# Kernel optimization log

Measured on AMD Instinct MI355X. Metric: run time of the kernel, lower is better.

## Reference

```python
import jax, jax.numpy as jnp
import numpy as np

B, S, D = 1, 2048, 1024
H, HD = 16, 64          # attention heads, head dim
DFF = 4096              # ffn hidden
IH, ID = 4, 64          # indexer heads / dim ('baseline' strategy)
TOP_K = 64
ROPE_BASE = 10000.0
LN_EPS = 1e-5


def setup_inputs() -> dict:
    key = jax.random.key(0)
    ks = jax.random.split(key, 12)
    g = lambda k, shape: (jax.random.normal(k, shape, dtype=jnp.float32) * 0.02)
    return {
        "x": jax.random.normal(ks[0], (B, S, D), dtype=jnp.float32),
        "w_qkv": g(ks[1], (D, 3 * D)),
        "w_o": g(ks[2], (D, D)),
        "ffn_w1": g(ks[3], (D, DFF)),
        "ffn_b1": jnp.zeros((DFF,), jnp.float32),
        "ffn_w2": g(ks[4], (DFF, D)),
        "ffn_b2": jnp.zeros((D,), jnp.float32),
        "ln1_g": jnp.ones((D,), jnp.float32),
        "ln1_b": jnp.zeros((D,), jnp.float32),
        "ln2_g": jnp.ones((D,), jnp.float32),
        "ln2_b": jnp.zeros((D,), jnp.float32),
        "idx_wq": g(ks[5], (D, IH * ID)),
        "idx_wk": g(ks[6], (D, ID)),
        "idx_ww": g(ks[7], (D, IH)),
    }


def _layernorm(x, g, b):
    m = jnp.mean(x, axis=-1, keepdims=True)
    v = jnp.var(x, axis=-1, keepdims=True)
    return (x - m) * jax.lax.rsqrt(v + LN_EPS) * g + b


def _rope(x):  # x: [B,S,H,HD], torchtune interleaved-pair convention
    half = HD // 2
    theta = 1.0 / (ROPE_BASE ** (jnp.arange(0, HD, 2, dtype=jnp.float32) / HD))  # [half]
    ang = jnp.arange(S, dtype=jnp.float32)[:, None] * theta                      # [S,half]
    cos = jnp.cos(ang)[None, :, None, :]
    sin = jnp.sin(ang)[None, :, None, :]
    xp = x.reshape(*x.shape[:-1], half, 2)
    x0, x1 = xp[..., 0], xp[..., 1]
    out = jnp.stack([x0 * cos - x1 * sin, x1 * cos + x0 * sin], axis=-1)
    return out.reshape(x.shape)


def reference(x, w_qkv, w_o, ffn_w1, ffn_b1, ffn_w2, ffn_b2,
              ln1_g, ln1_b, ln2_g, ln2_b, idx_wq, idx_wk, idx_ww):
    norm_x = _layernorm(x, ln1_g, ln1_b)

    qkv = norm_x @ w_qkv                              # [B,S,3D]
    q, k, v = jnp.split(qkv, 3, axis=-1)
    q = _rope(q.reshape(B, S, H, HD))
    k = _rope(k.reshape(B, S, H, HD))
    v = v.reshape(B, S, H, HD)

    # Lightning-style indexer: I[t,s] = sum_h w[t,h] * relu(q_i[t,h] . k_i[s])
    qi = (norm_x @ idx_wq).reshape(B, S, IH, ID)      # [B,S,IH,ID]
    ki = norm_x @ idx_wk                              # [B,S,ID]
    wi = norm_x @ idx_ww                              # [B,S,IH]
    qk = jnp.einsum("bthd,bsd->bths", qi, ki)         # [B,S,IH,S]
    index_scores = jnp.einsum("bth,bths->bts", wi, jax.nn.relu(qk))  # [B,S,S]

    # causal top-k token selection -> boolean mask
    causal = jnp.tril(jnp.ones((S, S), dtype=bool))
    masked_scores = jnp.where(causal, index_scores, -jnp.inf)
    _, topk_idx = jax.lax.top_k(masked_scores, TOP_K)  # [B,S,K]
    b_ix = jnp.arange(B)[:, None, None]
    q_ix = jnp.arange(S)[None, :, None]
    mask = jnp.zeros((B, S, S), dtype=bool).at[b_ix, q_ix, topk_idx].set(True)
    mask = mask & causal                               # [B,S,S]

    # masked SDPA
    logits = jnp.einsum("bqhd,bkhd->bhqk", q, k) / np.sqrt(HD)
    logits = jnp.where(mask[:, None, :, :], logits, -jnp.inf)
    attn = jax.nn.softmax(logits, axis=-1)
    attn_out = jnp.einsum("bhqk,bkhd->bqhd", attn, v).reshape(B, S, D)
    x = x + attn_out @ w_o

    h = _layernorm(x, ln2_g, ln2_b)
    ffn = jax.nn.gelu(h @ ffn_w1 + ffn_b1, approximate=False) @ ffn_w2 + ffn_b2
    return x + ffn
```

## Files before the change

### kernel.cpp

```cpp
#include <hip/hip_runtime.h>
#include <math.h>

#define S_LEN 2048
#define D_MODEL 1024
#define NHEAD 16
#define HDIM 64
#define DFF 4096
#define IH 4
#define IDM 64
#define TOPK 64
#define NIDX 336

typedef float f32x4 __attribute__((ext_vector_type(4)));
typedef short bf16x8 __attribute__((ext_vector_type(8)));

__device__ __forceinline__ unsigned short f2bf(float f) {
    unsigned u = __builtin_bit_cast(unsigned, f);
    u += 0x7fff + ((u >> 16) & 1);
    return (unsigned short)(u >> 16);
}
__device__ __forceinline__ float bf2f(unsigned short us) {
    return __builtin_bit_cast(float, (unsigned)us << 16);
}

__device__ __forceinline__ float gelu_exact(float v) {
    return 0.5f * v * (1.f + erff(v * 0.70710678118654752f));
}

__device__ __forceinline__ void gl_lds16(const void* g, void* l) {
    __builtin_amdgcn_global_load_lds(
        (const __attribute__((address_space(1))) void*)g,
        (__attribute__((address_space(3))) void*)l, 16, 0, 0);
}

__global__ __launch_bounds__(256) void ln_kernel(const float* __restrict__ x,
    const float* __restrict__ g, const float* __restrict__ b,
    float* __restrict__ outf, unsigned short* __restrict__ outb)
{
    int row = blockIdx.x, tid = threadIdx.x;
    const float4 v = *(const float4*)(x + (size_t)row * D_MODEL + tid * 4);
    float s = v.x + v.y + v.z + v.w;
    float ss = v.x * v.x + v.y * v.y + v.z * v.z + v.w * v.w;
    int lane = tid & 63, wv = tid >> 6;
    for (int o = 32; o; o >>= 1) { s += __shfl_xor(s, o); ss += __shfl_xor(ss, o); }
    __shared__ float rs[4], rss[4];
    if (lane == 0) { rs[wv] = s; rss[wv] = ss; }
    __syncthreads();
    float S = rs[0] + rs[1] + rs[2] + rs[3];
    float SS = rss[0] + rss[1] + rss[2] + rss[3];
    float mean = S * (1.f / D_MODEL);
    float var = SS * (1.f / D_MODEL) - mean * mean;
    float r = rsqrtf(var + 1e-5f);
    float4 gv = *(const float4*)(g + tid * 4);
    float4 bv = *(const float4*)(b + tid * 4);
    float4 o4;
    o4.x = (v.x - mean) * r * gv.x + bv.x;
    o4.y = (v.y - mean) * r * gv.y + bv.y;
    o4.z = (v.z - mean) * r * gv.z + bv.z;
    o4.w = (v.w - mean) * r * gv.w + bv.w;
    if (outf) *(float4*)(outf + (size_t)row * D_MODEL + tid * 4) = o4;
    if (outb) {
        ushort4 u4 = { f2bf(o4.x), f2bf(o4.y), f2bf(o4.z), f2bf(o4.w) };
        *(ushort4*)(outb + (size_t)row * D_MODEL + tid * 4) = u4;
    }
}

__global__ __launch_bounds__(256) void wtrans_kernel(const float* __restrict__ in,
    unsigned short* __restrict__ out, int K, int N)
{
    __shared__ float t[32][33];
    int k0 = blockIdx.y * 32, n0 = blockIdx.x * 32;
    int tid = threadIdx.x;
    int r = tid >> 5, c = tid & 31;
#pragma unroll
    for (int p = 0; p < 4; ++p)
        t[r + p * 8][c] = in[(size_t)(k0 + r + p * 8) * N + n0 + c];
    __syncthreads();
#pragma unroll
    for (int p = 0; p < 4; ++p)
        out[(size_t)(n0 + r + p * 8) * K + k0 + c] = f2bf(t[c][r + p * 8]);
}

__global__ __launch_bounds__(256) void wpack_kernel(const float* __restrict__ wq,
    const float* __restrict__ wk, const float* __restrict__ ww, float* __restrict__ Wc)
{
    int idx = blockIdx.x * 256 + threadIdx.x;
    if (idx >= D_MODEL * NIDX) return;
    int r = idx / NIDX, c = idx % NIDX;
    float v = 0.f;
    if (c < 256) v = wq[r * 256 + c];
    else if (c < 320) v = wk[r * 64 + (c - 256)];
    else if (c < 324) v = ww[r * 4 + (c - 320)];
    Wc[idx] = v;
}

__global__ __launch_bounds__(256) void gemm_bf16_n64(
    const unsigned short* __restrict__ A, const unsigned short* __restrict__ Bt,
    float* __restrict__ C, unsigned short* __restrict__ Cb,
    const float* __restrict__ bias, const float* __restrict__ R,
    int M, int N, int K, int act,
    float* __restrict__ P, int kchunk)
{
    __shared__ __attribute__((aligned(16))) unsigned short As[2][128 * 32];
    __shared__ __attribute__((aligned(16))) unsigned short Bs[2][64 * 32];
    int tid = threadIdx.x;
    int bm = blockIdx.y * 128, bn = blockIdx.x * 64;
    int wid = tid >> 6, lane = tid & 63;
    int wm = wid * 32;
    const unsigned short* Ab = A + (size_t)bm * K;
    const unsigned short* Bb = Bt + (size_t)bn * K;
    f32x4 acc[2][4];
#pragma unroll
    for (int i = 0; i < 2; ++i)
#pragma unroll
        for (int j = 0; j < 4; ++j)
            acc[i][j] = (f32x4){0.f, 0.f, 0.f, 0.f};

    int kbeg = blockIdx.z * kchunk;
    int kend = kbeg + kchunk;
    int fr = lane & 15;
    int srow = tid >> 2;
    int cels = (((tid & 3) ^ (srow & 3)) << 3);
    int dste = tid * 8;
    int selm = (((lane >> 4) ^ (fr & 3)) << 3);

    gl_lds16(Ab + (size_t)srow * K + kbeg + cels, &As[0][dste]);
    gl_lds16(Ab + (size_t)(srow + 64) * K + kbeg + cels, &As[0][dste + 2048]);
    gl_lds16(Bb + (size_t)srow * K + kbeg + cels, &Bs[0][dste]);
    __syncthreads();

    int cur = 0;
    for (int k0 = kbeg; k0 < kend; k0 += 32) {
        int nxt = k0 + 32;
        if (nxt < kend) {
            gl_lds16(Ab + (size_t)srow * K + nxt + cels, &As[cur ^ 1][dste]);
            gl_lds16(Ab + (size_t)(srow + 64) * K + nxt + cels, &As[cur ^ 1][dste + 2048]);
            gl_lds16(Bb + (size_t)srow * K + nxt + cels, &Bs[cur ^ 1][dste]);
        }
        bf16x8 af[2], bfv[4];
#pragma unroll
        for (int mi = 0; mi < 2; ++mi)
            af[mi] = *(const bf16x8*)&As[cur][(wm + mi * 16 + fr) * 32 + selm];
#pragma unroll
        for (int ni = 0; ni < 4; ++ni)
            bfv[ni] = *(const bf16x8*)&Bs[cur][(ni * 16 + fr) * 32 + selm];
#pragma unroll
        for (int mi = 0; mi < 2; ++mi)
#pragma unroll
            for (int ni = 0; ni < 4; ++ni)
                acc[mi][ni] = __builtin_amdgcn_mfma_f32_16x16x32_bf16(
                    af[mi], bfv[ni], acc[mi][ni], 0, 0, 0);
        __syncthreads();
        cur ^= 1;
    }
    int cl = lane & 15, rh = (lane >> 4) * 4;
    if (P) {
        float* Pz = P + (size_t)blockIdx.z * M * N;
#pragma unroll
        for (int mi = 0; mi < 2; ++mi)
#pragma unroll
            for (int ni = 0; ni < 4; ++ni) {
                int col = bn + ni * 16 + cl;
#pragma unroll
                for (int r = 0; r < 4; ++r) {
                    int row = bm + wm + mi * 16 + rh + r;
                    Pz[(size_t)row * N + col] = acc[mi][ni][r];
                }
            }
        return;
    }
#pragma unroll
    for (int mi = 0; mi < 2; ++mi) {
#pragma unroll
        for (int ni = 0; ni < 4; ++ni) {
            int col = bn + ni * 16 + cl;
            float bv = bias ? bias[col] : 0.f;
#pragma unroll
            for (int r = 0; r < 4; ++r) {
                int row = bm + wm + mi * 16 + rh + r;
                float v = acc[mi][ni][r] + bv;
                if (act) v = gelu_exact(v);
                size_t off = (size_t)row * N + col;
                if (R) v += R[off];
                if (C) C[off] = v;
                if (Cb) Cb[off] = f2bf(v);
            }
        }
    }
}

__global__ __launch_bounds__(256) void kreduce_kernel(const float* __restrict__ P,
    int nslice, float* __restrict__ C, const float* __restrict__ bias,
    const float* __restrict__ R, int M, int N)
{
    size_t total4 = (size_t)M * N / 4;
    size_t stride = (size_t)gridDim.x * 256;
    for (size_t i4 = blockIdx.x * 256 + threadIdx.x; i4 < total4; i4 += stride) {
        size_t off = i4 * 4;
        float4 v = *(const float4*)(P + off);
        for (int z = 1; z < nslice; ++z) {
            float4 p = *(const float4*)(P + (size_t)z * M * N + off);
            v.x += p.x; v.y += p.y; v.z += p.z; v.w += p.w;
        }
        if (bias) {
            float4 b4 = *(const float4*)(bias + (off % N));
            v.x += b4.x; v.y += b4.y; v.z += b4.z; v.w += b4.w;
        }
        if (R) {
            float4 r4 = *(const float4*)(R + off);
            v.x += r4.x; v.y += r4.y; v.z += r4.z; v.w += r4.w;
        }
        *(float4*)(C + off) = v;
    }
}

__global__ __launch_bounds__(256) void gemm64(const float* __restrict__ A,
    const float* __restrict__ B, float* __restrict__ C,
    int M, int N, int K,
    float* __restrict__ P, int kchunk)
{
    __shared__ float As[16][68];
    __shared__ float Bs[16][68];
    int tid = threadIdx.x;
    int bm = blockIdx.y, bn = blockIdx.x;
    int tx = tid & 15, ty = tid >> 4;
    int arow = tid >> 2;
    int acol = (tid & 3) << 2;
    int brow = tid >> 4;
    int bcol = (tid & 15) << 2;
    const float* Abase = A + (size_t)(bm * 64 + arow) * K + acol;
    float c[4][4] = {};
    int kbeg = blockIdx.z * kchunk;
    int kend = kbeg + kchunk;
    for (int k0 = kbeg; k0 < kend; k0 += 16) {
        float4 av = *(const float4*)(Abase + k0);
        As[acol + 0][arow] = av.x;
        As[acol + 1][arow] = av.y;
        As[acol + 2][arow] = av.z;
        As[acol + 3][arow] = av.w;
        int gcol = bn * 64 + bcol;
        const float* Bb = B + (size_t)(k0 + brow) * N;
        float4 bv;
        if (gcol + 3 < N) {
            bv = *(const float4*)(Bb + gcol);
        } else {
            bv.x = (gcol + 0 < N) ? Bb[gcol + 0] : 0.f;
            bv.y = (gcol + 1 < N) ? Bb[gcol + 1] : 0.f;
            bv.z = (gcol + 2 < N) ? Bb[gcol + 2] : 0.f;
            bv.w = (gcol + 3 < N) ? Bb[gcol + 3] : 0.f;
        }
        *(float4*)&Bs[brow][bcol] = bv;
        __syncthreads();
#pragma unroll
        for (int kk = 0; kk < 16; ++kk) {
            float4 a4 = *(const float4*)&As[kk][ty * 4];
            float4 b4 = *(const float4*)&Bs[kk][tx * 4];
            float av4[4] = { a4.x, a4.y, a4.z, a4.w };
            float bv4[4] = { b4.x, b4.y, b4.z, b4.w };
#pragma unroll
            for (int i = 0; i < 4; ++i)
#pragma unroll
                for (int j = 0; j < 4; ++j)
                    c[i][j] += av4[i] * bv4[j];
        }
        __syncthreads();
    }
    float* Out = P ? (P + (size_t)blockIdx.z * M * N) : C;
#pragma unroll
    for (int i = 0; i < 4; ++i) {
        int row = bm * 64 + ty * 4 + i;
#pragma unroll
        for (int j = 0; j < 4; ++j) {
            int col = bn * 64 + tx * 4 + j;
            if (col < N)
                Out[(size_t)row * N + col] = c[i][j];
        }
    }
}

__global__ __launch_bounds__(256) void rope_table_kernel(float* __restrict__ ct, float* __restrict__ st)
{
    int g = blockIdx.x * 256 + threadIdx.x;
    int t = g >> 5, i = g & 31;
    float theta = powf(10000.f, -(float)i / 32.f);
    float ang = (float)t * theta;
    ct[g] = cosf(ang);
    st[g] = sinf(ang);
}

__global__ __launch_bounds__(512) void rope_pack_kernel(
    const unsigned short* __restrict__ qkvb,
    const float* __restrict__ ct, const float* __restrict__ st,
    unsigned short* __restrict__ Qb, unsigned short* __restrict__ Kb,
    unsigned short* __restrict__ Vb)
{
    int t = blockIdx.x, tid = threadIdx.x;
    int h = tid >> 5, i = tid & 31;
    float c = ct[t * 32 + i], s = st[t * 32 + i];
    const unsigned short* base = qkvb + (size_t)t * (3 * D_MODEL);
    ushort2 q2 = *(const ushort2*)(base + h * HDIM + 2 * i);
    float q0 = bf2f(q2.x), q1 = bf2f(q2.y);
    ushort2 qo = { f2bf(q0 * c - q1 * s), f2bf(q1 * c + q0 * s) };
    *(ushort2*)(Qb + (size_t)t * D_MODEL + h * HDIM + 2 * i) = qo;
    ushort2 k2 = *(const ushort2*)(base + D_MODEL + h * HDIM + 2 * i);
    float k0 = bf2f(k2.x), k1 = bf2f(k2.y);
    ushort2 ko = { f2bf(k0 * c - k1 * s), f2bf(k1 * c + k0 * s) };
    *(ushort2*)(Kb + ((size_t)h * S_LEN + t) * HDIM + 2 * i) = ko;
    ushort2 v2 = *(const ushort2*)(base + 2 * D_MODEL + 2 * tid);
    int vh = tid >> 5, vd = (2 * tid) & 63;
    *(ushort2*)(Vb + ((size_t)vh * S_LEN + t) * HDIM + vd) = v2;
}

__global__ __launch_bounds__(256) void scores_kernel(const float* __restrict__ QIW,
    float* __restrict__ scores)
{
    int t0 = blockIdx.y * 32, s0 = blockIdx.x * 32;
    if (s0 > t0 + 31) return;
    __shared__ float qis[32][256];
    __shared__ float kis[32][65];
    __shared__ float wis[32][4];
    int tid = threadIdx.x;
#pragma unroll
    for (int l = 0; l < 8; ++l) {
        int idx = l * 256 + tid;
        int r = idx >> 6, c = (idx & 63) << 2;
        *(float4*)&qis[r][c] = *(const float4*)(QIW + (size_t)(t0 + r) * NIDX + c);
    }
#pragma unroll
    for (int l = 0; l < 8; ++l) {
        int idx = l * 256 + tid;
        int r = idx >> 6, c = idx & 63;
        kis[r][c] = QIW[(size_t)(s0 + r) * NIDX + 256 + c];
    }
    if (tid < 32) *(float4*)&wis[tid][0] = *(const float4*)(QIW + (size_t)(t0 + tid) * NIDX + 320);
    __syncthreads();
    int sl = tid & 31;
    int tb = (tid >> 5) * 4;
    float acc[4] = { 0.f, 0.f, 0.f, 0.f };
#pragma unroll
    for (int h = 0; h < 4; ++h) {
        float dots[4] = { 0.f, 0.f, 0.f, 0.f };
        for (int d = 0; d < 64; ++d) {
            float kv = kis[sl][d];
#pragma unroll
            for (int i = 0; i < 4; ++i)
                dots[i] += qis[tb + i][h * 64 + d] * kv;
        }
#pragma unroll
        for (int i = 0; i < 4; ++i)
            acc[i] += wis[tb + i][h] * fmaxf(dots[i], 0.f);
    }
#pragma unroll
    for (int i = 0; i < 4; ++i)
        scores[(size_t)(t0 + tb + i) * S_LEN + s0 + sl] = acc[i];
}

__global__ __launch_bounds__(256) void topk_kernel(const float* __restrict__ scores,
    int* __restrict__ topidx, int* __restrict__ topcnt)
{
    int t = blockIdx.x, tid = threadIdx.x;
    int n = t + 1;
    if (n <= TOPK) {
        if (tid < n) topidx[t * TOPK + tid] = tid;
        if (tid == 0) topcnt[t] = n;
        return;
    }
    __shared__ unsigned sc[S_LEN];
    __shared__ unsigned hist[256];
    __shared__ int selbin_s;
    __shared__ int cnt_out;
    __shared__ unsigned wsum[4];
    for (int j = tid; j < n; j += 256) {
        unsigned u = __builtin_bit_cast(unsigned, scores[(size_t)t * S_LEN + j]);
        sc[j] = (u & 0x80000000u) ? ~u : (u | 0x80000000u);
    }
    if (tid == 0) cnt_out = 0;
    int lane = tid & 63, wv = tid >> 6;
    unsigned prefix = 0;
    int kk = TOPK;
#pragma unroll
    for (int round = 0; round < 4; ++round) {
        int shift_pref = 32 - 8 * round;
        int shift_bin = 24 - 8 * round;
        hist[tid] = 0;
        __syncthreads();
        for (int j = tid; j < n; j += 256) {
            unsigned v = sc[j];
            if ((((unsigned long long)(v ^ prefix)) >> shift_pref) == 0)
                atomicAdd(&hist[(v >> shift_bin) & 0xff], 1u);
        }
        __syncthreads();
        if (wv == 0) {
            unsigned h0 = hist[4 * lane], h1 = hist[4 * lane + 1];
            unsigned h2 = hist[4 * lane + 2], h3 = hist[4 * lane + 3];
            unsigned s3 = h3, s2 = h2 + s3, s1 = h1 + s2, s0 = h0 + s1;
            unsigned acc = s0;
            for (int off = 1; off < 64; off <<= 1) {
                unsigned o = __shfl_down(acc, off);
                if (lane + off < 64) acc += o;
            }
            unsigned above = acc - s0;
            hist[4 * lane]     = s0 + above;
            hist[4 * lane + 1] = s1 + above;
            hist[4 * lane + 2] = s2 + above;
            hist[4 * lane + 3] = s3 + above;
        }
        __syncthreads();
        {
            unsigned sufb = hist[tid];
            unsigned sufn = (tid < 255) ? hist[tid + 1] : 0u;
            if (sufb >= (unsigned)kk && sufn < (unsigned)kk)
                selbin_s = tid;
        }
        __syncthreads();
        int b = selbin_s;
        unsigned above = (b < 255) ? hist[b + 1] : 0u;
        kk -= (int)above;
        prefix |= ((unsigned)b) << shift_bin;
        __syncthreads();
    }
    unsigned T = prefix;
    int chunk = (n + 255) >> 8;
    int jb = tid * chunk;
    int je = jb + chunk; if (je > n) je = n;
    int ties = 0;
    for (int j = jb; j < je; ++j) {
        unsigned v = sc[j];
        if (v > T) { int o = atomicAdd(&cnt_out, 1); topidx[t * TOPK + o] = j; }
        else if (v == T) ++ties;
    }
    unsigned inc = (unsigned)ties;
    for (int off = 1; off < 64; off <<= 1) {
        unsigned o = __shfl_up(inc, off);
        if (lane >= off) inc += o;
    }
    if (lane == 63) wsum[wv] = inc;
    __syncthreads();
    unsigned woff = 0;
    for (int w = 0; w < wv; ++w) woff += wsum[w];
    int rank = (int)(woff + inc) - ties;
    for (int j = jb; j < je && rank < kk; ++j) {
        if (sc[j] == T) {
            int o = atomicAdd(&cnt_out, 1);
            topidx[t * TOPK + o] = j;
            ++rank;
        }
    }
    if (tid == 0) topcnt[t] = TOPK;
}

__global__ __launch_bounds__(256) void attn_kernel(
    const unsigned short* __restrict__ Qb, const unsigned short* __restrict__ Kb,
    const unsigned short* __restrict__ Vb,
    const int* __restrict__ topidx, const int* __restrict__ topcnt,
    unsigned short* __restrict__ out)
{
    int t = blockIdx.x, tid = threadIdx.x;
    __shared__ int sel[TOPK];
    if (tid < TOPK) sel[tid] = topidx[t * TOPK + tid];
    __syncthreads();
    int cnt = topcnt[t];
    int lane = tid & 63, wv = tid >> 6;
    int h = blockIdx.y * 4 + wv;
    int klo = lane >> 3, oct = lane & 7;
    int rows[8];
    bool valid[8];
#pragma unroll
    for (int kg = 0; kg < 8; ++kg) {
        int k = kg * 8 + klo;
        valid[kg] = (k < cnt);
        rows[kg] = sel[valid[kg] ? k : 0];
    }
    bf16x8 q8 = *(const bf16x8*)(Qb + (size_t)t * D_MODEL + h * HDIM + oct * 8);
    float qf[8];
#pragma unroll
    for (int e = 0; e < 8; ++e) qf[e] = bf2f((unsigned short)q8[e]);

    const unsigned short* kbase = Kb + (size_t)h * S_LEN * HDIM + oct * 8;
    float p[8];
#pragma unroll
    for (int kg = 0; kg < 8; ++kg) {
        bf16x8 k8 = *(const bf16x8*)(kbase + (size_t)rows[kg] * HDIM);
        float d = 0.f;
#pragma unroll
        for (int e = 0; e < 8; ++e)
            d += bf2f((unsigned short)k8[e]) * qf[e];
        d += __shfl_xor(d, 1);
        d += __shfl_xor(d, 2);
        d += __shfl_xor(d, 4);
        p[kg] = valid[kg] ? d * 0.125f : -INFINITY;
    }
    float m = p[0];
#pragma unroll
    for (int kg = 1; kg < 8; ++kg) m = fmaxf(m, p[kg]);
    m = fmaxf(m, __shfl_xor(m, 8));
    m = fmaxf(m, __shfl_xor(m, 16));
    m = fmaxf(m, __shfl_xor(m, 32));
    float sum = 0.f;
#pragma unroll
    for (int kg = 0; kg < 8; ++kg) { p[kg] = __expf(p[kg] - m); sum += p[kg]; }
    sum += __shfl_xor(sum, 8);
    sum += __shfl_xor(sum, 16);
    sum += __shfl_xor(sum, 32);
    float rs = 1.f / sum;
    const unsigned short* vbase = Vb + (size_t)h * S_LEN * HDIM + oct * 8;
    float facc[8] = {};
#pragma unroll
    for (int kg = 0; kg < 8; ++kg) {
        bf16x8 v8 = *(const bf16x8*)(vbase + (size_t)rows[kg] * HDIM);
        float pw = p[kg] * rs;
#pragma unroll
        for (int e = 0; e < 8; ++e)
            facc[e] += pw * bf2f((unsigned short)v8[e]);
    }
#pragma unroll
    for (int e = 0; e < 8; ++e) {
        facc[e] += __shfl_xor(facc[e], 8);
        facc[e] += __shfl_xor(facc[e], 16);
        facc[e] += __shfl_xor(facc[e], 32);
    }
    if (klo == 0) {
        ushort4 o0 = { f2bf(facc[0]), f2bf(facc[1]), f2bf(facc[2]), f2bf(facc[3]) };
        ushort4 o1 = { f2bf(facc[4]), f2bf(facc[5]), f2bf(facc[6]), f2bf(facc[7]) };
        *(ushort4*)(out + (size_t)t * D_MODEL + h * HDIM + oct * 8) = o0;
        *(ushort4*)(out + (size_t)t * D_MODEL + h * HDIM + oct * 8 + 4) = o1;
    }
}

extern "C" void kernel_launch(void* const* d_in, const int* in_sizes, int n_in,
                              void* d_out, int out_size, void* d_ws, size_t ws_size,
                              hipStream_t stream)
{
    const float* x      = (const float*)d_in[0];
    const float* w_qkv  = (const float*)d_in[1];
    const float* w_o    = (const float*)d_in[2];
    const float* ffn_w1 = (const float*)d_in[3];
    const float* ffn_b1 = (const float*)d_in[4];
    const float* ffn_w2 = (const float*)d_in[5];
    const float* ffn_b2 = (const float*)d_in[6];
    const float* ln1_g  = (const float*)d_in[7];
    const float* ln1_b  = (const float*)d_in[8];
    const float* ln2_g  = (const float*)d_in[9];
    const float* ln2_b  = (const float*)d_in[10];
    const float* idx_wq = (const float*)d_in[11];
    const float* idx_wk = (const float*)d_in[12];
    const float* idx_ww = (const float*)d_in[13];
    float* outp = (float*)d_out;

    const size_t MB = 1ull << 20;
    char* ws = (char*)d_ws;
    float*          normx    = (float*)(ws + 0);
    unsigned short* attno_bf = (unsigned short*)(ws + 0);
    float*          Pf2      = (float*)(ws + 0);
    unsigned short* normx_bf = (unsigned short*)(ws + 8 * MB);
    unsigned short* h2_bf    = normx_bf;
    unsigned short* qkv_bf   = (unsigned short*)(ws + 12 * MB);
    int*            topidx   = (int*)(ws + 12 * MB);
    int*            topcnt   = (int*)(ws + 12 * MB + 512 * 1024);
    unsigned short* wqkv_t   = (unsigned short*)(ws + 24 * MB);
    unsigned short* wo_t     = (unsigned short*)(ws + 30 * MB);
    unsigned short* w1_t     = (unsigned short*)(ws + 32 * MB);
    unsigned short* w2_t     = (unsigned short*)(ws + 40 * MB);
    unsigned short* Qb       = (unsigned short*)(ws + 48 * MB);
    unsigned short* Kb       = (unsigned short*)(ws + 52 * MB);
    unsigned short* Vb       = (unsigned short*)(ws + 56 * MB);
    float*          ctab     = (float*)(ws + 60 * MB);
    float*          stab     = (float*)(ws + 60 * MB + 256 * 1024);
    float*          P_idx    = (float*)(ws + 60 * MB);
    float*          scoresb  = (float*)(ws + 60 * MB);
    float*          Pwo      = (float*)(ws + 60 * MB);
    unsigned short* ffn1_bf  = (unsigned short*)(ws + 60 * MB);
    float*          QIW      = (float*)(ws + 76 * MB);
    float*          Wc       = (float*)(ws + 79 * MB);

    dim3 blk256(256);
    auto g64n = [](int N, int M) { return dim3(N / 64, M / 128); };

    ln_kernel<<<S_LEN, blk256, 0, stream>>>(x, ln1_g, ln1_b, normx, normx_bf);
    rope_table_kernel<<<(S_LEN * 32) / 256, blk256, 0, stream>>>(ctab, stab);
    wtrans_kernel<<<dim3(3 * D_MODEL / 32, D_MODEL / 32), blk256, 0, stream>>>(w_qkv, wqkv_t, D_MODEL, 3 * D_MODEL);
    wtrans_kernel<<<dim3(D_MODEL / 32, D_MODEL / 32), blk256, 0, stream>>>(w_o, wo_t, D_MODEL, D_MODEL);
    wtrans_kernel<<<dim3(DFF / 32, D_MODEL / 32), blk256, 0, stream>>>(ffn_w1, w1_t, D_MODEL, DFF);
    wtrans_kernel<<<dim3(D_MODEL / 32, DFF / 32), blk256, 0, stream>>>(ffn_w2, w2_t, DFF, D_MODEL);
    wpack_kernel<<<(D_MODEL * NIDX + 255) / 256, blk256, 0, stream>>>(idx_wq, idx_wk, idx_ww, Wc);
    gemm_bf16_n64<<<g64n(3 * D_MODEL, S_LEN), blk256, 0, stream>>>(normx_bf, wqkv_t,
        nullptr, qkv_bf, nullptr, nullptr, S_LEN, 3 * D_MODEL, D_MODEL, 0, nullptr, D_MODEL);
    rope_pack_kernel<<<S_LEN, dim3(512), 0, stream>>>(qkv_bf, ctab, stab, Qb, Kb, Vb);
    gemm64<<<dim3((NIDX + 63) / 64, S_LEN / 64, 4), blk256, 0, stream>>>(normx, Wc,
        nullptr, S_LEN, NIDX, D_MODEL, P_idx, D_MODEL / 4);
    kreduce_kernel<<<1024, blk256, 0, stream>>>(P_idx, 4, QIW, nullptr, nullptr, S_LEN, NIDX);
    scores_kernel<<<dim3(64, 64), blk256, 0, stream>>>(QIW, scoresb);
    topk_kernel<<<S_LEN, blk256, 0, stream>>>(scoresb, topidx, topcnt);
    attn_kernel<<<dim3(S_LEN, 4), blk256, 0, stream>>>(Qb, Kb, Vb, topidx, topcnt, attno_bf);
    gemm_bf16_n64<<<dim3(D_MODEL / 64, S_LEN / 128, 2), blk256, 0, stream>>>(attno_bf, wo_t,
        nullptr, nullptr, nullptr, nullptr, S_LEN, D_MODEL, D_MODEL, 0, Pwo, D_MODEL / 2);
    kreduce_kernel<<<1024, blk256, 0, stream>>>(Pwo, 2, outp, nullptr, x, S_LEN, D_MODEL);
    ln_kernel<<<S_LEN, blk256, 0, stream>>>(outp, ln2_g, ln2_b, nullptr, h2_bf);
    gemm_bf16_n64<<<g64n(DFF, S_LEN), blk256, 0, stream>>>(h2_bf, w1_t,
        nullptr, ffn1_bf, ffn_b1, nullptr, S_LEN, DFF, D_MODEL, 1, nullptr, D_MODEL);
    gemm_bf16_n64<<<dim3(D_MODEL / 64, S_LEN / 128, 4), blk256, 0, stream>>>(ffn1_bf, w2_t,
        nullptr, nullptr, nullptr, nullptr, S_LEN, D_MODEL, DFF, 0, Pf2, DFF / 4);
    kreduce_kernel<<<1024, blk256, 0, stream>>>(Pf2, 4, outp, ffn_b2, outp, S_LEN, D_MODEL);
}
```

Baseline: 276.4 us.

## Retile indexer scores kernel to 64x64 blocks with 4x4 register tiles

The indexer scores kernel moves from 32x32 tiles, where each thread computes 4 outputs, to 64x64 tiles where each thread computes a 4x4 register block. Q and K are stored transposed in padded shared memory so each inner step reads two float4 vectors and does 16 FMAs. K is loaded once and Q one head at a time. This cuts shared-memory traffic per FMA and allows vectorized stores. In exchange, fewer blocks launch and the causal tile skipping is coarser.

```diff
diff --git a/kernel.cpp b/kernel.cpp
--- a/kernel.cpp
+++ b/kernel.cpp
@@ -314,45 +314,64 @@
 __global__ __launch_bounds__(256) void scores_kernel(const float* __restrict__ QIW,
     float* __restrict__ scores)
 {
-    int t0 = blockIdx.y * 32, s0 = blockIdx.x * 32;
-    if (s0 > t0 + 31) return;
-    __shared__ float qis[32][256];
-    __shared__ float kis[32][65];
-    __shared__ float wis[32][4];
+    int t0 = blockIdx.y * 64, s0 = blockIdx.x * 64;
+    if (s0 > t0 + 63) return;
+    __shared__ float qit[64][68];
+    __shared__ float kit[64][68];
+    __shared__ float wis[64][4];
     int tid = threadIdx.x;
-#pragma unroll
-    for (int l = 0; l < 8; ++l) {
-        int idx = l * 256 + tid;
-        int r = idx >> 6, c = (idx & 63) << 2;
-        *(float4*)&qis[r][c] = *(const float4*)(QIW + (size_t)(t0 + r) * NIDX + c);
-    }
-#pragma unroll
-    for (int l = 0; l < 8; ++l) {
-        int idx = l * 256 + tid;
-        int r = idx >> 6, c = idx & 63;
-        kis[r][c] = QIW[(size_t)(s0 + r) * NIDX + 256 + c];
-    }
-    if (tid < 32) *(float4*)&wis[tid][0] = *(const float4*)(QIW + (size_t)(t0 + tid) * NIDX + 320);
-    __syncthreads();
-    int sl = tid & 31;
-    int tb = (tid >> 5) * 4;
-    float acc[4] = { 0.f, 0.f, 0.f, 0.f };
+    int tx = tid & 15, ty = tid >> 4;
+    int lr = tid & 63;
+    int cseg = tid >> 6;
+    if (tid < 64) {
+        float4 w4 = *(const float4*)(QIW + (size_t)(t0 + tid) * NIDX + 320);
+        wis[tid][0] = w4.x; wis[tid][1] = w4.y; wis[tid][2] = w4.z; wis[tid][3] = w4.w;
+    }
+    float acc[4][4] = {};
 #pragma unroll
     for (int h = 0; h < 4; ++h) {
-        float dots[4] = { 0.f, 0.f, 0.f, 0.f };
+        __syncthreads();
+        const float* qrow = QIW + (size_t)(t0 + lr) * NIDX + h * 64 + cseg * 16;
+        const float* krow = QIW + (size_t)(s0 + lr) * NIDX + 256 + cseg * 16;
+#pragma unroll
+        for (int q4 = 0; q4 < 4; ++q4) {
+            int d = cseg * 16 + q4 * 4;
+            float4 v = *(const float4*)(qrow + q4 * 4);
+            qit[d + 0][lr] = v.x; qit[d + 1][lr] = v.y;
+            qit[d + 2][lr] = v.z; qit[d + 3][lr] = v.w;
+            if (h == 0) {
+                float4 u = *(const float4*)(krow + q4 * 4);
+                kit[d + 0][lr] = u.x; kit[d + 1][lr] = u.y;
+                kit[d + 2][lr] = u.z; kit[d + 3][lr] = u.w;
+            }
+        }
+        __syncthreads();
+        float dot[4][4] = {};
+#pragma unroll 8
         for (int d = 0; d < 64; ++d) {
-            float kv = kis[sl][d];
+            float4 a4 = *(const float4*)&qit[d][ty * 4];
+            float4 b4 = *(const float4*)&kit[d][tx * 4];
+            float av[4] = { a4.x, a4.y, a4.z, a4.w };
+            float bv[4] = { b4.x, b4.y, b4.z, b4.w };
 #pragma unroll
             for (int i = 0; i < 4; ++i)
-                dots[i] += qis[tb + i][h * 64 + d] * kv;
-        }
-#pragma unroll
-        for (int i = 0; i < 4; ++i)
-            acc[i] += wis[tb + i][h] * fmaxf(dots[i], 0.f);
-    }
-#pragma unroll
-    for (int i = 0; i < 4; ++i)
-        scores[(size_t)(t0 + tb + i) * S_LEN + s0 + sl] = acc[i];
+#pragma unroll
+                for (int j = 0; j < 4; ++j)
+                    dot[i][j] += av[i] * bv[j];
+        }
+#pragma unroll
+        for (int i = 0; i < 4; ++i) {
+            float w = wis[ty * 4 + i][h];
+#pragma unroll
+            for (int j = 0; j < 4; ++j)
+                acc[i][j] += w * fmaxf(dot[i][j], 0.f);
+        }
+    }
+#pragma unroll
+    for (int i = 0; i < 4; ++i) {
+        float4 o4 = { acc[i][0], acc[i][1], acc[i][2], acc[i][3] };
+        *(float4*)&scores[(size_t)(t0 + ty * 4 + i) * S_LEN + s0 + tx * 4] = o4;
+    }
 }
 
 __global__ __launch_bounds__(256) void topk_kernel(const float* __restrict__ scores,
@@ -589,7 +608,7 @@
     gemm64<<<dim3((NIDX + 63) / 64, S_LEN / 64, 4), blk256, 0, stream>>>(normx, Wc,
         nullptr, S_LEN, NIDX, D_MODEL, P_idx, D_MODEL / 4);
     kreduce_kernel<<<1024, blk256, 0, stream>>>(P_idx, 4, QIW, nullptr, nullptr, S_LEN, NIDX);
-    scores_kernel<<<dim3(64, 64), blk256, 0, stream>>>(QIW, scoresb);
+    scores_kernel<<<dim3(32, 32), blk256, 0, stream>>>(QIW, scoresb);
     topk_kernel<<<S_LEN, blk256, 0, stream>>>(scoresb, topidx, topcnt);
     attn_kernel<<<dim3(S_LEN, 4), blk256, 0, stream>>>(Qb, Kb, Vb, topidx, topcnt, attno_bf);
     gemm_bf16_n64<<<dim3(D_MODEL / 64, S_LEN / 128, 2), blk256, 0, stream>>>(attno_bf, wo_t,
```

Result: no change. 272.2 us (-1.5%).
